# Optimization experiments

Hardware: AMD Instinct MI355X
Metric: run time of the kernel (lower is better)

## Reference

```python
import jax, jax.numpy as jnp
import numpy as np

B, L, E, H = 2, 2048, 1024, 16
D = E // H  # head dim = 64


def setup_inputs() -> dict:
    key = jax.random.key(0)
    ks = jax.random.split(key, 10)
    s = 0.02
    return {
        "xt": jax.random.normal(ks[0], (B, L, E), jnp.float32),
        "xs": jax.random.normal(ks[1], (B, L, E), jnp.float32),
        "Wt": jax.random.normal(ks[2], (E, 3 * E), jnp.float32) * s,  # t_attn weight (x @ Wt)
        "bt": jnp.zeros((3 * E,), jnp.float32),
        "Ws": jax.random.normal(ks[3], (E, 2 * E), jnp.float32) * s,  # s_attn weight
        "bs": jnp.zeros((2 * E,), jnp.float32),
        "Wc": jax.random.normal(ks[4], (E, E), jnp.float32) * s,      # c_proj weight
        "bc": jnp.zeros((E,), jnp.float32),
        "lam_ts": jnp.ones((1,), jnp.float32),
        "lam_st": jnp.ones((1,), jnp.float32),
        "lam_ss": jnp.ones((1,), jnp.float32),
    }


def _heads(x):
    # (B, L, E) -> (B, H, L, D)
    return x.reshape(B, L, H, D).transpose(0, 2, 1, 3)


def reference(xt, xs, Wt, bt, Ws, bs, Wc, bc, lam_ts, lam_st, lam_ss):
    qt, kt, vt = jnp.split(xt @ Wt + bt, 3, axis=2)
    qs, ks = jnp.split(xs @ Ws + bs, 2, axis=2)
    qt, kt, vt, qs, ks = map(_heads, (qt, kt, vt, qs, ks))

    # 4-way disentangled scores; fuse the 4 matmuls into 2 by combining keys:
    # qt@kt^T + lam_ts*qt@ks^T = qt @ (kt + lam_ts*ks)^T
    # lam_st*qs@kt^T + lam_ss*qs@ks^T = qs @ (lam_st*kt + lam_ss*ks)^T
    k1 = kt + lam_ts[0] * ks
    k2 = lam_st[0] * kt + lam_ss[0] * ks
    att = (jnp.einsum('bhqd,bhkd->bhqk', qt, k1)
           + jnp.einsum('bhqd,bhkd->bhqk', qs, k2)) * (1.0 / np.sqrt(D))
    att = jax.nn.softmax(att, axis=-1)
    y = jnp.einsum('bhqk,bhkd->bhqd', att, vt)  # (B, H, L, D)
    y = y.transpose(0, 2, 1, 3).reshape(B, L, E)
    return y @ Wc + bc
```

## Files before the change

kernel.cpp:

```cpp
#include <hip/hip_runtime.h>
#include <math.h>

#define LQ 2048
#define EQ 1024
#define M_ROWS 4096
#define BH 32

typedef _Float16 f16x8 __attribute__((ext_vector_type(8)));
typedef _Float16 f16x4 __attribute__((ext_vector_type(4)));
typedef float f32x4 __attribute__((ext_vector_type(4)));
typedef float f32x16 __attribute__((ext_vector_type(16)));

#define QSCALE 0.1803368801111204f

__device__ __forceinline__ void async_ld16(const _Float16* g, _Float16* l) {
  __builtin_amdgcn_global_load_lds(
      (const __attribute__((address_space(1))) unsigned int*)g,
      (__attribute__((address_space(3))) unsigned int*)l, 16, 0, 0);
}

__global__ __launch_bounds__(256) void convert_x(
    const float* __restrict__ xt, const float* __restrict__ xs,
    _Float16* __restrict__ xt16, _Float16* __restrict__ xs16) {
  int i = blockIdx.x * 256 + threadIdx.x;
  const float* s; _Float16* d; size_t off;
  if (i < 524288) { s = xt; d = xt16; off = (size_t)i * 8; }
  else            { s = xs; d = xs16; off = (size_t)(i - 524288) * 8; }
  float4 a = *(const float4*)&s[off];
  float4 b = *(const float4*)&s[off + 4];
  f16x8 h;
  h[0] = (_Float16)a.x; h[1] = (_Float16)a.y; h[2] = (_Float16)a.z; h[3] = (_Float16)a.w;
  h[4] = (_Float16)b.x; h[5] = (_Float16)b.y; h[6] = (_Float16)b.z; h[7] = (_Float16)b.w;
  *(f16x8*)&d[off] = h;
}

__global__ __launch_bounds__(256) void transpose_w(
    const float* __restrict__ Wt, const float* __restrict__ Ws,
    const float* __restrict__ Wc,
    _Float16* __restrict__ WtT, _Float16* __restrict__ WsT,
    _Float16* __restrict__ WcT) {
  __shared__ float T[32][33];
  int tx = threadIdx.x & 31, ty = threadIdx.x >> 5;
  int c0 = blockIdx.x * 32;
  int k0 = blockIdx.y * 32;
  const float* W; _Float16* D; int Nw, cl;
  if (c0 < 3072)      { W = Wt; D = WtT; Nw = 3072; cl = c0; }
  else if (c0 < 5120) { W = Ws; D = WsT; Nw = 2048; cl = c0 - 3072; }
  else                { W = Wc; D = WcT; Nw = 1024; cl = c0 - 5120; }
#pragma unroll
  for (int j = 0; j < 4; ++j)
    T[ty + j * 8][tx] = W[(size_t)(k0 + ty + j * 8) * Nw + cl + tx];
  __syncthreads();
#pragma unroll
  for (int j = 0; j < 4; ++j)
    D[(size_t)(cl + ty + j * 8) * 1024 + k0 + tx] = (_Float16)T[tx][ty + j * 8];
}

__global__ __launch_bounds__(256) void gemm_bt(
    const _Float16* __restrict__ A, const _Float16* __restrict__ Bm,
    const float* __restrict__ bias,
    float* __restrict__ outf, _Float16* __restrict__ q16,
    _Float16* __restrict__ k16, _Float16* __restrict__ v16,
    const float* __restrict__ lam_ts, const float* __restrict__ lam_st,
    const float* __restrict__ lam_ss,
    int N, int mode) {
  __shared__ _Float16 Al[128 * 32];
  __shared__ _Float16 Bl[128 * 32];

  const int tid = threadIdx.x;
  const int w = tid >> 6;
  const int lane = tid & 63;
  const int quad = lane >> 4;
  const int l15 = lane & 15;
  const int wm = w >> 1, wn = w & 1;
  const int m0 = blockIdx.y * 128;
  const int n0 = blockIdx.x * 128;

  const int srow = lane >> 2;
  const int schunk = ((lane & 3) ^ ((lane >> 3) & 3)) * 8;

  float lts = 0.f, lst = 0.f, lss = 0.f;
  if (mode == 1) { lts = lam_ts[0]; lst = lam_st[0]; lss = lam_ss[0]; }

  f32x4 acc[4][4];
#pragma unroll
  for (int mb = 0; mb < 4; ++mb)
#pragma unroll
    for (int nb = 0; nb < 4; ++nb) acc[mb][nb] = (f32x4){0.f, 0.f, 0.f, 0.f};

  const int key = (l15 >> 1) & 3;

  for (int kt = 0; kt < 1024; kt += 32) {
    __syncthreads();
#pragma unroll
    for (int i = 0; i < 2; ++i) {
      int rt = w * 32 + i * 16;
      async_ld16(&A[(size_t)(m0 + rt + srow) * 1024 + kt + schunk], &Al[rt * 32]);
      async_ld16(&Bm[(size_t)(n0 + rt + srow) * 1024 + kt + schunk], &Bl[rt * 32]);
    }
    __syncthreads();

    f16x8 af[4], bf[4];
    const int pc = (quad ^ key) * 8;
#pragma unroll
    for (int mb = 0; mb < 4; ++mb)
      af[mb] = *(f16x8*)&Al[(wm * 64 + mb * 16 + l15) * 32 + pc];
#pragma unroll
    for (int nb = 0; nb < 4; ++nb)
      bf[nb] = *(f16x8*)&Bl[(wn * 64 + nb * 16 + l15) * 32 + pc];
#pragma unroll
    for (int mb = 0; mb < 4; ++mb)
#pragma unroll
      for (int nb = 0; nb < 4; ++nb)
        acc[mb][nb] = __builtin_amdgcn_mfma_f32_16x16x32_f16(af[mb], bf[nb], acc[mb][nb], 0, 0, 0);
  }

#pragma unroll
  for (int mb = 0; mb < 4; ++mb)
#pragma unroll
    for (int nb = 0; nb < 4; ++nb)
#pragma unroll
      for (int r = 0; r < 4; ++r) {
        int row = m0 + wm * 64 + mb * 16 + quad * 4 + r;
        int col = n0 + wn * 64 + nb * 16 + l15;
        float val = acc[mb][nb][r] + bias[col];
        if (mode == 2) {
          outf[(size_t)row * 1024 + col] = val;
        } else {
          int bb = row >> 11, ll = row & 2047;
          int which = col >> 10, e = col & 1023;
          int hh = e >> 6, dd = e & 63;
          size_t rowhd = (size_t)(bb * 16 + hh) * 2048 + ll;
          if (mode == 0) {
            if (which == 0)      q16[rowhd * 128 + dd] = (_Float16)(val * QSCALE);
            else if (which == 1) k16[rowhd * 128 + dd] = (_Float16)val;
            else                 v16[((size_t)(bb * 16 + hh) * 64 + dd) * 2048 + ll] = (_Float16)val;
          } else {
            if (which == 0) {
              q16[rowhd * 128 + 64 + dd] = (_Float16)(val * QSCALE);
            } else {
              float ktv = (float)k16[rowhd * 128 + dd];
              float ksv = val;
              k16[rowhd * 128 + dd]      = (_Float16)(ktv + lts * ksv);
              k16[rowhd * 128 + 64 + dd] = (_Float16)(lst * ktv + lss * ksv);
            }
          }
        }
      }
}

__global__ __launch_bounds__(256, 2) void flash_attn_mfma(
    const _Float16* __restrict__ qcat, const _Float16* __restrict__ kcat,
    const _Float16* __restrict__ vT, _Float16* __restrict__ y) {
  const int bh = blockIdx.y;
  const int qt0 = blockIdx.x * 128;
  const int b = bh >> 4, h = bh & 15;
  const _Float16* Qg = qcat + (size_t)bh * LQ * 128;
  const _Float16* Kg = kcat + (size_t)bh * LQ * 128;
  const _Float16* Vg = vT + (size_t)bh * 64 * LQ;

  __shared__ _Float16 Ksh[64 * 128];
  __shared__ _Float16 Vsh[64 * 64];
  __shared__ _Float16 Psh[4 * 32 * 72];

  const int tid = threadIdx.x;
  const int w = tid >> 6;
  const int lane = tid & 63;
  const int half = lane >> 5;
  const int l31 = lane & 31;

  f16x8 qf[8];
#pragma unroll
  for (int db = 0; db < 8; ++db)
    qf[db] = *(const f16x8*)&Qg[(size_t)(qt0 + w * 32 + l31) * 128 + db * 16 + half * 8];

  float m_i = -INFINITY;
  float l_i = 0.f;
  f32x16 O[2];
#pragma unroll
  for (int nt = 0; nt < 2; ++nt)
#pragma unroll
    for (int r = 0; r < 16; ++r) O[nt][r] = 0.f;

  _Float16* Pw = &Psh[w * 32 * 72];

  for (int t = 0; t < LQ; t += 64) {
    __syncthreads();

#pragma unroll
    for (int a = 0; a < 4; ++a) {
      int row = w * 16 + a * 4 + (lane >> 4);
      int sc = (lane & 15) ^ (row & 7);
      async_ld16(&Kg[(size_t)(t + row) * 128 + sc * 8], &Ksh[(w * 16 + a * 4) * 128]);
    }
#pragma unroll
    for (int a = 0; a < 2; ++a) {
      int row = w * 16 + a * 8 + (lane >> 3);
      int sc = (lane & 7) ^ (row & 7);
      async_ld16(&Vg[(size_t)row * LQ + t + sc * 8], &Vsh[(w * 16 + a * 8) * 64]);
    }
    __syncthreads();

    f32x16 S[2];
#pragma unroll
    for (int kb = 0; kb < 2; ++kb)
#pragma unroll
      for (int r = 0; r < 16; ++r) S[kb][r] = 0.f;
#pragma unroll
    for (int db = 0; db < 8; ++db) {
      const int pc = ((db * 2 + half) ^ (lane & 7)) * 8;
      f16x8 af[2];
#pragma unroll
      for (int kb = 0; kb < 2; ++kb)
        af[kb] = *(f16x8*)&Ksh[(kb * 32 + l31) * 128 + pc];
#pragma unroll
      for (int kb = 0; kb < 2; ++kb)
        S[kb] = __builtin_amdgcn_mfma_f32_32x32x16_f16(af[kb], qf[db], S[kb], 0, 0, 0);
    }

    float mx = -INFINITY;
#pragma unroll
    for (int kb = 0; kb < 2; ++kb)
#pragma unroll
      for (int r = 0; r < 16; ++r) mx = fmaxf(mx, S[kb][r]);
    mx = fmaxf(mx, __shfl_xor(mx, 32));
    float m_new = fmaxf(m_i, mx);
    float alpha = __builtin_amdgcn_exp2f(m_i - m_new);
    float s = 0.f;
#pragma unroll
    for (int kb = 0; kb < 2; ++kb)
#pragma unroll
      for (int r = 0; r < 16; ++r) {
        float p = __builtin_amdgcn_exp2f(S[kb][r] - m_new);
        S[kb][r] = p;
        s += p;
      }
    s += __shfl_xor(s, 32);
    l_i = l_i * alpha + s;
    m_i = m_new;

#pragma unroll
    for (int kb = 0; kb < 2; ++kb)
#pragma unroll
      for (int rg = 0; rg < 4; ++rg) {
        f16x4 p4;
#pragma unroll
        for (int i = 0; i < 4; ++i) p4[i] = (_Float16)S[kb][rg * 4 + i];
        *(f16x4*)&Pw[l31 * 72 + kb * 32 + rg * 8 + half * 4] = p4;
      }

#pragma unroll
    for (int nt = 0; nt < 2; ++nt)
#pragma unroll
      for (int r = 0; r < 16; ++r) O[nt][r] *= alpha;

#pragma unroll
    for (int kb = 0; kb < 4; ++kb) {
      f16x8 pb = *(f16x8*)&Pw[l31 * 72 + kb * 16 + half * 8];
      f16x8 av[2];
#pragma unroll
      for (int nt = 0; nt < 2; ++nt) {
        int dim = nt * 32 + l31;
        int pc = ((kb * 2 + half) ^ (dim & 7)) * 8;
        av[nt] = *(f16x8*)&Vsh[dim * 64 + pc];
      }
#pragma unroll
      for (int nt = 0; nt < 2; ++nt)
        O[nt] = __builtin_amdgcn_mfma_f32_32x32x16_f16(av[nt], pb, O[nt], 0, 0, 0);
    }
  }

  float inv = 1.f / l_i;
  int qrow = qt0 + w * 32 + l31;
#pragma unroll
  for (int nt = 0; nt < 2; ++nt)
#pragma unroll
    for (int rg = 0; rg < 4; ++rg) {
      f16x4 o4;
#pragma unroll
      for (int i = 0; i < 4; ++i) o4[i] = (_Float16)(O[nt][rg * 4 + i] * inv);
      int dim = nt * 32 + rg * 8 + half * 4;
      *(f16x4*)&y[((size_t)b * LQ + qrow) * EQ + h * 64 + dim] = o4;
    }
}

extern "C" void kernel_launch(void* const* d_in, const int* in_sizes, int n_in,
                              void* d_out, int out_size, void* d_ws, size_t ws_size,
                              hipStream_t stream) {
  const float* xt = (const float*)d_in[0];
  const float* xs = (const float*)d_in[1];
  const float* Wt = (const float*)d_in[2];
  const float* bt = (const float*)d_in[3];
  const float* Ws = (const float*)d_in[4];
  const float* bs = (const float*)d_in[5];
  const float* Wc = (const float*)d_in[6];
  const float* bc = (const float*)d_in[7];
  const float* lam_ts = (const float*)d_in[8];
  const float* lam_st = (const float*)d_in[9];
  const float* lam_ss = (const float*)d_in[10];
  float* out = (float*)d_out;

  _Float16* w16 = (_Float16*)d_ws;
  _Float16* xt16 = w16;
  _Float16* xs16 = xt16 + 4194304;
  _Float16* WtT  = xs16 + 4194304;
  _Float16* WsT  = WtT + 3145728;
  _Float16* WcT  = WsT + 2097152;
  _Float16* qcat = WcT + 1048576;
  _Float16* kcat = qcat + 8388608;
  _Float16* vbufT = kcat + 8388608;
  _Float16* ybuf = vbufT + 4194304;

  convert_x<<<4096, 256, 0, stream>>>(xt, xs, xt16, xs16);
  transpose_w<<<dim3(192, 32), 256, 0, stream>>>(Wt, Ws, Wc, WtT, WsT, WcT);
  gemm_bt<<<dim3(24, 32), 256, 0, stream>>>(
      xt16, WtT, bt, nullptr, qcat, kcat, vbufT, nullptr, nullptr, nullptr, 3072, 0);
  gemm_bt<<<dim3(16, 32), 256, 0, stream>>>(
      xs16, WsT, bs, nullptr, qcat, kcat, nullptr, lam_ts, lam_st, lam_ss, 2048, 1);
  flash_attn_mfma<<<dim3(16, 32), 256, 0, stream>>>(qcat, kcat, vbufT, ybuf);
  gemm_bt<<<dim3(8, 32), 256, 0, stream>>>(
      ybuf, WcT, bc, out, nullptr, nullptr, nullptr, nullptr, nullptr, nullptr, 1024, 2);
}
```

Baseline: 292.7 us.

## Double-buffer K/V tiles in flash attention and compute V transposed in QKV GEMM

The attention kernel now ping-pongs between two LDS buffers for K and V. The next tile's async global-to-LDS loads are issued before computing on the current tile, with one barrier per sub-step instead of two, so load latency overlaps MFMA work. The xt projection GEMM now computes the V block as W_v^T · x^T through extra grid rows, so V^T stores are coalesced along the sequence instead of scattered column writes. The cost is doubled LDS per block, which may reduce occupancy below the two-blocks-per-CU launch bound, and a more complex GEMM index path.

```diff
diff --git a/kernel.cpp b/kernel.cpp
--- a/kernel.cpp
+++ b/kernel.cpp
@@ -63,7 +63,7 @@
     _Float16* __restrict__ k16, _Float16* __restrict__ v16,
     const float* __restrict__ lam_ts, const float* __restrict__ lam_st,
     const float* __restrict__ lam_ss,
-    int N, int mode) {
+    int mode) {
   __shared__ _Float16 Al[128 * 32];
   __shared__ _Float16 Bl[128 * 32];
 
@@ -73,8 +73,21 @@
   const int quad = lane >> 4;
   const int l15 = lane & 15;
   const int wm = w >> 1, wn = w & 1;
-  const int m0 = blockIdx.y * 128;
+
+  const _Float16* Ab = A;
+  const _Float16* Bb = Bm;
+  int m0 = blockIdx.y * 128;
   const int n0 = blockIdx.x * 128;
+  int bsel = 0;
+  bool vpath = false;
+  if (mode == 0 && blockIdx.y >= 32) {
+    int by2 = blockIdx.y - 32;
+    bsel = by2 >> 3;
+    m0 = (by2 & 7) * 128;
+    Ab = Bm + (size_t)2048 * 1024;
+    Bb = A + (size_t)bsel * 2048 * 1024;
+    vpath = true;
+  }
 
   const int srow = lane >> 2;
   const int schunk = ((lane & 3) ^ ((lane >> 3) & 3)) * 8;
@@ -95,8 +108,8 @@
 #pragma unroll
     for (int i = 0; i < 2; ++i) {
       int rt = w * 32 + i * 16;
-      async_ld16(&A[(size_t)(m0 + rt + srow) * 1024 + kt + schunk], &Al[rt * 32]);
-      async_ld16(&Bm[(size_t)(n0 + rt + srow) * 1024 + kt + schunk], &Bl[rt * 32]);
+      async_ld16(&Ab[(size_t)(m0 + rt + srow) * 1024 + kt + schunk], &Al[rt * 32]);
+      async_ld16(&Bb[(size_t)(n0 + rt + srow) * 1024 + kt + schunk], &Bl[rt * 32]);
     }
     __syncthreads();
 
@@ -123,26 +136,30 @@
       for (int r = 0; r < 4; ++r) {
         int row = m0 + wm * 64 + mb * 16 + quad * 4 + r;
         int col = n0 + wn * 64 + nb * 16 + l15;
-        float val = acc[mb][nb][r] + bias[col];
-        if (mode == 2) {
-          outf[(size_t)row * 1024 + col] = val;
+        if (vpath) {
+          float val = acc[mb][nb][r] + bias[2048 + row];
+          v16[(size_t)(bsel * 1024 + row) * 2048 + col] = (_Float16)val;
         } else {
-          int bb = row >> 11, ll = row & 2047;
-          int which = col >> 10, e = col & 1023;
-          int hh = e >> 6, dd = e & 63;
-          size_t rowhd = (size_t)(bb * 16 + hh) * 2048 + ll;
-          if (mode == 0) {
-            if (which == 0)      q16[rowhd * 128 + dd] = (_Float16)(val * QSCALE);
-            else if (which == 1) k16[rowhd * 128 + dd] = (_Float16)val;
-            else                 v16[((size_t)(bb * 16 + hh) * 64 + dd) * 2048 + ll] = (_Float16)val;
+          float val = acc[mb][nb][r] + bias[col];
+          if (mode == 2) {
+            outf[(size_t)row * 1024 + col] = val;
           } else {
-            if (which == 0) {
-              q16[rowhd * 128 + 64 + dd] = (_Float16)(val * QSCALE);
+            int bb = row >> 11, ll = row & 2047;
+            int which = col >> 10, e = col & 1023;
+            int hh = e >> 6, dd = e & 63;
+            size_t rowhd = (size_t)(bb * 16 + hh) * 2048 + ll;
+            if (mode == 0) {
+              if (which == 0) q16[rowhd * 128 + dd] = (_Float16)(val * QSCALE);
+              else            k16[rowhd * 128 + dd] = (_Float16)val;
             } else {
-              float ktv = (float)k16[rowhd * 128 + dd];
-              float ksv = val;
-              k16[rowhd * 128 + dd]      = (_Float16)(ktv + lts * ksv);
-              k16[rowhd * 128 + 64 + dd] = (_Float16)(lst * ktv + lss * ksv);
+              if (which == 0) {
+                q16[rowhd * 128 + 64 + dd] = (_Float16)(val * QSCALE);
+              } else {
+                float ktv = (float)k16[rowhd * 128 + dd];
+                float ksv = val;
+                k16[rowhd * 128 + dd]      = (_Float16)(ktv + lts * ksv);
+                k16[rowhd * 128 + 64 + dd] = (_Float16)(lst * ktv + lss * ksv);
+              }
             }
           }
         }
@@ -159,8 +176,10 @@
   const _Float16* Kg = kcat + (size_t)bh * LQ * 128;
   const _Float16* Vg = vT + (size_t)bh * 64 * LQ;
 
-  __shared__ _Float16 Ksh[64 * 128];
-  __shared__ _Float16 Vsh[64 * 64];
+  __shared__ _Float16 Ksh0[64 * 128];
+  __shared__ _Float16 Ksh1[64 * 128];
+  __shared__ _Float16 Vsh0[64 * 64];
+  __shared__ _Float16 Vsh1[64 * 64];
   __shared__ _Float16 Psh[4 * 32 * 72];
 
   const int tid = threadIdx.x;
@@ -184,23 +203,22 @@
 
   _Float16* Pw = &Psh[w * 32 * 72];
 
-  for (int t = 0; t < LQ; t += 64) {
-    __syncthreads();
-
+  auto dma = [&](int t, _Float16* Kd, _Float16* Vd) {
 #pragma unroll
     for (int a = 0; a < 4; ++a) {
       int row = w * 16 + a * 4 + (lane >> 4);
       int sc = (lane & 15) ^ (row & 7);
-      async_ld16(&Kg[(size_t)(t + row) * 128 + sc * 8], &Ksh[(w * 16 + a * 4) * 128]);
+      async_ld16(&Kg[(size_t)(t + row) * 128 + sc * 8], &Kd[(w * 16 + a * 4) * 128]);
     }
 #pragma unroll
     for (int a = 0; a < 2; ++a) {
       int row = w * 16 + a * 8 + (lane >> 3);
       int sc = (lane & 7) ^ (row & 7);
-      async_ld16(&Vg[(size_t)row * LQ + t + sc * 8], &Vsh[(w * 16 + a * 8) * 64]);
-    }
-    __syncthreads();
-
+      async_ld16(&Vg[(size_t)row * LQ + t + sc * 8], &Vd[(w * 16 + a * 8) * 64]);
+    }
+  };
+
+  auto compute = [&](const _Float16* Ks, const _Float16* Vs) {
     f32x16 S[2];
 #pragma unroll
     for (int kb = 0; kb < 2; ++kb)
@@ -212,7 +230,7 @@
       f16x8 af[2];
 #pragma unroll
       for (int kb = 0; kb < 2; ++kb)
-        af[kb] = *(f16x8*)&Ksh[(kb * 32 + l31) * 128 + pc];
+        af[kb] = *(const f16x8*)&Ks[(kb * 32 + l31) * 128 + pc];
 #pragma unroll
       for (int kb = 0; kb < 2; ++kb)
         S[kb] = __builtin_amdgcn_mfma_f32_32x32x16_f16(af[kb], qf[db], S[kb], 0, 0, 0);
@@ -256,18 +274,28 @@
 
 #pragma unroll
     for (int kb = 0; kb < 4; ++kb) {
-      f16x8 pb = *(f16x8*)&Pw[l31 * 72 + kb * 16 + half * 8];
+      f16x8 pb = *(const f16x8*)&Pw[l31 * 72 + kb * 16 + half * 8];
       f16x8 av[2];
 #pragma unroll
       for (int nt = 0; nt < 2; ++nt) {
         int dim = nt * 32 + l31;
         int pc = ((kb * 2 + half) ^ (dim & 7)) * 8;
-        av[nt] = *(f16x8*)&Vsh[dim * 64 + pc];
+        av[nt] = *(const f16x8*)&Vs[dim * 64 + pc];
       }
 #pragma unroll
       for (int nt = 0; nt < 2; ++nt)
         O[nt] = __builtin_amdgcn_mfma_f32_32x32x16_f16(av[nt], pb, O[nt], 0, 0, 0);
     }
+  };
+
+  dma(0, Ksh0, Vsh0);
+  for (int t = 0; t < LQ; t += 128) {
+    __syncthreads();
+    dma(t + 64, Ksh1, Vsh1);
+    compute(Ksh0, Vsh0);
+    __syncthreads();
+    if (t + 128 < LQ) dma(t + 128, Ksh0, Vsh0);
+    compute(Ksh1, Vsh1);
   }
 
   float inv = 1.f / l_i;
@@ -313,11 +341,11 @@
 
   convert_x<<<4096, 256, 0, stream>>>(xt, xs, xt16, xs16);
   transpose_w<<<dim3(192, 32), 256, 0, stream>>>(Wt, Ws, Wc, WtT, WsT, WcT);
-  gemm_bt<<<dim3(24, 32), 256, 0, stream>>>(
-      xt16, WtT, bt, nullptr, qcat, kcat, vbufT, nullptr, nullptr, nullptr, 3072, 0);
+  gemm_bt<<<dim3(16, 48), 256, 0, stream>>>(
+      xt16, WtT, bt, nullptr, qcat, kcat, vbufT, nullptr, nullptr, nullptr, 0);
   gemm_bt<<<dim3(16, 32), 256, 0, stream>>>(
-      xs16, WsT, bs, nullptr, qcat, kcat, nullptr, lam_ts, lam_st, lam_ss, 2048, 1);
+      xs16, WsT, bs, nullptr, qcat, kcat, nullptr, lam_ts, lam_st, lam_ss, 1);
   flash_attn_mfma<<<dim3(16, 32), 256, 0, stream>>>(qcat, kcat, vbufT, ybuf);
   gemm_bt<<<dim3(8, 32), 256, 0, stream>>>(
-      ybuf, WcT, bc, out, nullptr, nullptr, nullptr, nullptr, nullptr, nullptr, 1024, 2);
-}
+      ybuf, WcT, bc, out, nullptr, nullptr, nullptr, nullptr, nullptr, nullptr, 2);
+}
```

Measured after the change: 308.0 us. +5.2%, slower.
